# Kernel optimization log

Measured on AMD Instinct MI355X. Metric: run time of the kernel, lower is better.

## Reference

```python
import jax, jax.numpy as jnp
import numpy as np

B, C_LEN, Q_LEN, H = 32, 1024, 128, 512
NEG = -1e30  # effectively -inf for fp32 softmax


def setup_inputs() -> dict:
    key = jax.random.key(0)
    k1, k2, k3, k4, k5, k6 = jax.random.split(key, 6)
    C = jax.random.normal(k1, (B, C_LEN, H), dtype=jnp.float32)
    Q = jax.random.normal(k2, (B, Q_LEN, H), dtype=jnp.float32)
    C_mask = jax.random.randint(k3, (B, C_LEN), 0, 2, dtype=jnp.int32)
    Q_mask = jax.random.randint(k4, (B, Q_LEN), 0, 2, dtype=jnp.int32)
    # nn.Linear(3H, 1): weight [1, 3H], bias [1]; store as flat vector + scalar
    w = jax.random.normal(k5, (3 * H,), dtype=jnp.float32) * (1.0 / np.sqrt(3 * H))
    b = jax.random.normal(k6, (1,), dtype=jnp.float32) * 0.01
    return {"C": C, "Q": Q, "C_mask": C_mask, "Q_mask": Q_mask, "w": w, "b": b}


def reference(C, Q, C_mask, Q_mask, w, b):
    h = C.shape[-1]
    w1, w2, w3 = w[:h], w[h:2 * h], w[2 * h:]
    # Trilinear score decomposition (same math as Linear on cat(C, Q, C*Q)):
    # S[b,i,j] = C_i.w1 + Q_j.w2 + (C_i*w3).Q_j + bias
    S = (C @ w1)[:, :, None] + (Q @ w2)[:, None, :] \
        + jnp.einsum('bih,bjh->bij', C * w3, Q) + b[0]
    S_row = jax.nn.softmax(jnp.where(Q_mask[:, None, :] == 0, NEG, S), axis=2)
    S_col = jax.nn.softmax(jnp.where(C_mask[:, :, None] == 0, NEG, S), axis=1)
    A = jnp.einsum('bij,bjh->bih', S_row, Q)                     # [B, c_len, H]
    Bm = jnp.einsum('bij,bkj,bkh->bih', S_row, S_col, C)         # S_row @ S_col^T @ C
    return jnp.concatenate((C, A, C * A, C * Bm), axis=-1)       # [B, c_len, 4H]
```

## Files before the change

### kernel.cpp

```cpp
#include <hip/hip_runtime.h>
#include <hip/hip_bf16.h>
#include <math.h>

#define Bn 32
#define CL 1024
#define QL 128
#define Hh 512
#define NEGV (-1e30f)

typedef short bf16x8 __attribute__((ext_vector_type(8)));
typedef float f32x4 __attribute__((ext_vector_type(4)));

__device__ inline unsigned short f2bf(float x) {
  union { float f; unsigned u; } v; v.f = x;
  unsigned r = v.u + 0x7fff + ((v.u >> 16) & 1);
  return (unsigned short)(r >> 16);
}
__device__ inline unsigned packbf(float x, float y) {
  return (unsigned)f2bf(x) | ((unsigned)f2bf(y) << 16);
}

__global__ __launch_bounds__(256) void rowdot_kernel(
    const float* __restrict__ X, const float* __restrict__ w,
    const float* __restrict__ bias, float* __restrict__ out, int nrows) {
  int row = blockIdx.x * 4 + (threadIdx.x >> 6);
  int lane = threadIdx.x & 63;
  if (row >= nrows) return;
  const float* x = X + (size_t)row * Hh;
  float s = 0.f;
  for (int h = lane; h < Hh; h += 64) s += x[h] * w[h];
  for (int off = 32; off > 0; off >>= 1) s += __shfl_down(s, off, 64);
  if (lane == 0) out[row] = s + (bias ? bias[0] : 0.f);
}

__global__ __launch_bounds__(256) void prep_q_kernel(
    const float* __restrict__ Q, unsigned short* __restrict__ QT) {
  __shared__ float tile[QL * 65];
  int b = blockIdx.y, h0 = blockIdx.x * 64, t = threadIdx.x;
  const float* Qb = Q + (size_t)b * QL * Hh;
  unsigned* QTu = (unsigned*)QT + ((size_t)b * Hh + h0) * (QL / 2);
  for (int l = 0; l < 16; ++l) {
    int idx = t + l * 256; int c = idx & 31, j = idx >> 5;
    float2 v = *(const float2*)(Qb + (size_t)j * Hh + h0 + 2 * c);
    tile[j * 65 + 2 * c] = v.x;
    tile[j * 65 + 2 * c + 1] = v.y;
  }
  __syncthreads();
  for (int l = 0; l < 16; ++l) {
    int idx = t + l * 256; int jc = idx & 63, h = idx >> 6;
    QTu[(size_t)h * (QL / 2) + jc] =
        packbf(tile[(2 * jc) * 65 + h], tile[(2 * jc + 1) * 65 + h]);
  }
}

__global__ __launch_bounds__(256) void s_mfma_kernel(
    const float* __restrict__ C, const float* __restrict__ Q,
    const float* __restrict__ w3, const int* __restrict__ Qmask,
    const float* __restrict__ rc, const float* __restrict__ cq,
    float* __restrict__ S, unsigned short* __restrict__ Prow) {
  __shared__ unsigned sA[64 * 16];
  __shared__ unsigned sB[128 * 16];
  __shared__ float sW[Hh];
  __shared__ int qm[QL];
  int b = blockIdx.y, i0 = blockIdx.x * 64, t = threadIdx.x;
  if (t < QL) qm[t] = Qmask[b * QL + t];
  for (int l = t; l < Hh; l += 256) sW[l] = w3[l];
  __syncthreads();
  int lane = t & 63, w = t >> 6;
  int lanen = lane & 15, quad = lane >> 4;
  f32x4 acc[8];
  for (int nt = 0; nt < 8; ++nt) acc[nt] = (f32x4){0.f, 0.f, 0.f, 0.f};
  const float* Cb = C + ((size_t)b * CL + i0) * Hh;
  const float* Qb = Q + (size_t)b * QL * Hh;
  for (int k0 = 0; k0 < Hh; k0 += 32) {
    for (int l = 0; l < 4; ++l) {
      int idx = t + l * 256; int c = idx & 15, rr = idx >> 4;
      float2 v = *(const float2*)(Cb + (size_t)rr * Hh + k0 + c * 2);
      sA[rr * 16 + c] = packbf(v.x * sW[k0 + c * 2], v.y * sW[k0 + c * 2 + 1]);
    }
    for (int l = 0; l < 8; ++l) {
      int idx = t + l * 256; int c = idx & 15, j = idx >> 4;
      float2 v = *(const float2*)(Qb + (size_t)j * Hh + k0 + c * 2);
      sB[j * 16 + c] = packbf(v.x, v.y);
    }
    __syncthreads();
    bf16x8 a = *(const bf16x8*)(sA + (w * 16 + lanen) * 16 + quad * 4);
    for (int nt = 0; nt < 8; ++nt) {
      bf16x8 bb = *(const bf16x8*)(sB + (nt * 16 + lanen) * 16 + quad * 4);
      acc[nt] = __builtin_amdgcn_mfma_f32_16x16x32_bf16(a, bb, acc[nt], 0, 0, 0);
    }
    __syncthreads();
  }
  float cqv[8]; int qmv[8];
  for (int nt = 0; nt < 8; ++nt) {
    int j = nt * 16 + lanen;
    cqv[nt] = cq[b * QL + j]; qmv[nt] = qm[j];
  }
  int rowbase = i0 + w * 16 + quad * 4;
  for (int r = 0; r < 4; ++r) {
    int row = rowbase + r;
    float rcv = rc[b * CL + row];
    float vals[8], mv = -INFINITY;
    for (int nt = 0; nt < 8; ++nt) {
      float val = acc[nt][r] + rcv + cqv[nt];
      vals[nt] = val;
      mv = fmaxf(mv, qmv[nt] ? val : NEGV);
    }
    for (int off = 1; off < 16; off <<= 1) mv = fmaxf(mv, __shfl_xor(mv, off, 64));
    float ls = 0.f;
    for (int nt = 0; nt < 8; ++nt) ls += __expf((qmv[nt] ? vals[nt] : NEGV) - mv);
    for (int off = 1; off < 16; off <<= 1) ls += __shfl_xor(ls, off, 64);
    float linv = 1.f / ls;
    size_t base = ((size_t)b * CL + row) * QL;
    for (int nt = 0; nt < 8; ++nt) {
      int j = nt * 16 + lanen;
      S[base + j] = vals[nt];
      Prow[base + j] = f2bf(__expf((qmv[nt] ? vals[nt] : NEGV) - mv) * linv);
    }
  }
}

__global__ __launch_bounds__(256) void colstat1_kernel(
    const float* __restrict__ S, const int* __restrict__ Cmask,
    float* __restrict__ partm, float* __restrict__ partl) {
  __shared__ int cm[64];
  __shared__ float sm[QL], sl[QL];
  int b = blockIdx.y, chunk = blockIdx.x, t = threadIdx.x;
  int i0 = chunk * 64;
  if (t < 64) cm[t] = Cmask[b * CL + i0 + t];
  __syncthreads();
  int j = t & 127, ir = t >> 7;
  float m = -INFINITY, l = 0.f;
  const float* Sb = S + ((size_t)b * CL + i0) * QL;
  for (int i = ir; i < 64; i += 2) {
    float v = cm[i] ? Sb[(size_t)i * QL + j] : NEGV;
    float nm = fmaxf(m, v);
    l = l * __expf(m - nm) + __expf(v - nm);
    m = nm;
  }
  if (ir == 1) { sm[j] = m; sl[j] = l; }
  __syncthreads();
  if (ir == 0) {
    float m2 = sm[j], l2 = sl[j];
    float nm = fmaxf(m, m2);
    float L = l * __expf(m - nm) + l2 * __expf(m2 - nm);
    partm[(b * 16 + chunk) * QL + j] = nm;
    partl[(b * 16 + chunk) * QL + j] = L;
  }
}

__global__ __launch_bounds__(128) void colstat2_kernel(
    const float* __restrict__ partm, const float* __restrict__ partl,
    float* __restrict__ colm, float* __restrict__ colinv) {
  int b = blockIdx.x, j = threadIdx.x;
  float m = -INFINITY, L = 0.f;
  for (int c = 0; c < 16; ++c) {
    float m2 = partm[(b * 16 + c) * QL + j], l2 = partl[(b * 16 + c) * QL + j];
    float nm = fmaxf(m, m2);
    L = L * __expf(m - nm) + l2 * __expf(m2 - nm);
    m = nm;
  }
  colm[b * QL + j] = m;
  colinv[b * QL + j] = 1.f / L;
}

__global__ __launch_bounds__(256) void pcol_kernel(
    const float* __restrict__ S, const int* __restrict__ Cmask,
    const float* __restrict__ colm, const float* __restrict__ colinv,
    unsigned short* __restrict__ PT) {
  __shared__ float tile[64 * 129];
  __shared__ int cm[64];
  __shared__ float cmj[QL], civ[QL];
  int b = blockIdx.y, i0 = blockIdx.x * 64, t = threadIdx.x;
  if (t < 64) cm[t] = Cmask[b * CL + i0 + t];
  if (t >= 128) { int j = t - 128; cmj[j] = colm[b * QL + j]; civ[j] = colinv[b * QL + j]; }
  __syncthreads();
  const float* Sb = S + ((size_t)b * CL + i0) * QL;
  for (int l = 0; l < 32; ++l) {
    int idx = t + l * 256; int j = idx & 127, il = idx >> 7;
    float v = cm[il] ? Sb[(size_t)il * QL + j] : NEGV;
    tile[il * 129 + j] = __expf(v - cmj[j]) * civ[j];
  }
  __syncthreads();
  unsigned* PTu = (unsigned*)PT;
  for (int l = 0; l < 16; ++l) {
    int idx = t + l * 256; int c = idx & 31, j = idx >> 5;
    PTu[(((size_t)b * QL + j) * CL + i0) / 2 + c] =
        packbf(tile[(2 * c) * 129 + j], tile[(2 * c + 1) * 129 + j]);
  }
}

__global__ __launch_bounds__(256) void t_mfma_kernel(
    const float* __restrict__ C, const unsigned short* __restrict__ PT,
    unsigned short* __restrict__ TT) {
  __shared__ float ftile[32 * 33];
  __shared__ unsigned sA[32 * 16];
  __shared__ unsigned sB[128 * 16];
  int b = blockIdx.y, h0 = blockIdx.x * 32, t = threadIdx.x;
  int lane = t & 63, w = t >> 6;
  int lanen = lane & 15, quad = lane >> 4;
  int mw = w >> 1, nw = w & 1;
  f32x4 acc[4];
  for (int nt = 0; nt < 4; ++nt) acc[nt] = (f32x4){0.f, 0.f, 0.f, 0.f};
  const float* Cb = C + (size_t)b * CL * Hh;
  const unsigned* PTu = (const unsigned*)PT + ((size_t)b * QL * CL) / 2;
  for (int i0 = 0; i0 < CL; i0 += 32) {
    for (int l = 0; l < 4; ++l) {
      int idx = t + l * 256; int hh = idx & 31, ii = idx >> 5;
      ftile[ii * 33 + hh] = Cb[(size_t)(i0 + ii) * Hh + h0 + hh];
    }
    for (int l = 0; l < 8; ++l) {
      int idx = t + l * 256; int c = idx & 15, j = idx >> 4;
      sB[j * 16 + c] = PTu[(size_t)j * (CL / 2) + i0 / 2 + c];
    }
    __syncthreads();
    for (int l = 0; l < 2; ++l) {
      int idx = t + l * 256; int c = idx & 15, hh = idx >> 4;
      sA[hh * 16 + c] = packbf(ftile[(2 * c) * 33 + hh], ftile[(2 * c + 1) * 33 + hh]);
    }
    __syncthreads();
    bf16x8 a = *(const bf16x8*)(sA + (mw * 16 + lanen) * 16 + quad * 4);
    for (int nt = 0; nt < 4; ++nt) {
      bf16x8 bb = *(const bf16x8*)(sB + (nw * 64 + nt * 16 + lanen) * 16 + quad * 4);
      acc[nt] = __builtin_amdgcn_mfma_f32_16x16x32_bf16(a, bb, acc[nt], 0, 0, 0);
    }
    __syncthreads();
  }
  for (int nt = 0; nt < 4; ++nt)
    for (int r = 0; r < 4; ++r) {
      int h = h0 + mw * 16 + quad * 4 + r;
      int j = nw * 64 + nt * 16 + lanen;
      TT[((size_t)b * Hh + h) * QL + j] = f2bf(acc[nt][r]);
    }
}

__global__ __launch_bounds__(256) void out_mfma_kernel(
    const unsigned short* __restrict__ Prow, const unsigned short* __restrict__ TT,
    const unsigned short* __restrict__ QT, const float* __restrict__ C,
    float* __restrict__ out) {
  __shared__ unsigned smem[3 * 64 * 64];
  unsigned* sP = smem;
  unsigned* sQ = smem + 64 * 64;
  unsigned* sT = smem + 2 * 64 * 64;
  int b = blockIdx.z, i0 = blockIdx.y * 64, h0 = blockIdx.x * 64, t = threadIdx.x;
  int lane = t & 63, w = t >> 6;
  int lanen = lane & 15, quad = lane >> 4;
  const unsigned* Pu = (const unsigned*)Prow + ((size_t)b * CL + i0) * (QL / 2);
  const unsigned* Tu = (const unsigned*)TT + ((size_t)b * Hh + h0) * (QL / 2);
  const unsigned* Qu = (const unsigned*)QT + ((size_t)b * Hh + h0) * (QL / 2);
  for (int l = 0; l < 16; ++l) {
    int idx = t + l * 256; int c = idx & 63, rr = idx >> 6;
    int cs = c ^ ((rr & 7) << 2);
    sP[rr * 64 + cs] = Pu[(size_t)rr * 64 + c];
    sQ[rr * 64 + cs] = Qu[(size_t)rr * 64 + c];
    sT[rr * 64 + cs] = Tu[(size_t)rr * 64 + c];
  }
  __syncthreads();
  f32x4 accA[4], accB[4];
  for (int nt = 0; nt < 4; ++nt) {
    accA[nt] = (f32x4){0.f, 0.f, 0.f, 0.f};
    accB[nt] = (f32x4){0.f, 0.f, 0.f, 0.f};
  }
  for (int kk = 0; kk < 4; ++kk) {
    int arow = w * 16 + lanen;
    bf16x8 a = *(const bf16x8*)(sP + arow * 64 + ((kk * 16 + quad * 4) ^ ((arow & 7) << 2)));
    for (int nt = 0; nt < 4; ++nt) {
      int brow = nt * 16 + lanen;
      int boff = brow * 64 + ((kk * 16 + quad * 4) ^ ((brow & 7) << 2));
      bf16x8 bq = *(const bf16x8*)(sQ + boff);
      bf16x8 bt = *(const bf16x8*)(sT + boff);
      accA[nt] = __builtin_amdgcn_mfma_f32_16x16x32_bf16(a, bq, accA[nt], 0, 0, 0);
      accB[nt] = __builtin_amdgcn_mfma_f32_16x16x32_bf16(a, bt, accB[nt], 0, 0, 0);
    }
  }
  __syncthreads();
  float* fA = (float*)smem;
  float* fB = (float*)smem + 64 * 65;
  for (int nt = 0; nt < 4; ++nt)
    for (int r = 0; r < 4; ++r) {
      int iL = w * 16 + quad * 4 + r;
      int hL = nt * 16 + lanen;
      fA[iL * 65 + hL] = accA[nt][r];
      fB[iL * 65 + hL] = accB[nt][r];
    }
  __syncthreads();
  for (int rr = 0; rr < 16; ++rr) {
    int iL = w * 16 + rr;
    int i = i0 + iL;
    const float* Crow = C + ((size_t)b * CL + i) * Hh + h0;
    float* orow = out + ((size_t)b * CL + i) * (size_t)(4 * Hh) + h0;
    float cv = Crow[lane];
    float av = fA[iL * 65 + lane];
    float bv = fB[iL * 65 + lane];
    orow[lane] = cv;
    orow[Hh + lane] = av;
    orow[2 * Hh + lane] = cv * av;
    orow[3 * Hh + lane] = cv * bv;
  }
}

extern "C" void kernel_launch(void* const* d_in, const int* in_sizes, int n_in,
                              void* d_out, int out_size, void* d_ws, size_t ws_size,
                              hipStream_t stream) {
  const float* C = (const float*)d_in[0];
  const float* Q = (const float*)d_in[1];
  const int* Cmask = (const int*)d_in[2];
  const int* Qmask = (const int*)d_in[3];
  const float* w = (const float*)d_in[4];
  const float* bptr = (const float*)d_in[5];
  float* out = (float*)d_out;
  float* f = (float*)d_ws;

  float* rc     = f;
  float* cq     = f + 32768;
  float* colm   = f + 36864;
  float* colinv = f + 40960;
  float* partm  = f + 45056;
  float* partl  = f + 110592;
  float* S      = f + 176128;
  unsigned short* Prow = (unsigned short*)(f + 4370432);
  unsigned short* PT   = Prow + 4194304;
  unsigned short* TT   = PT + 4194304;
  unsigned short* QT   = TT + 2097152;

  rowdot_kernel<<<dim3((Bn * CL) / 4), 256, 0, stream>>>(C, w, nullptr, rc, Bn * CL);
  rowdot_kernel<<<dim3((Bn * QL) / 4), 256, 0, stream>>>(Q, w + Hh, bptr, cq, Bn * QL);
  prep_q_kernel<<<dim3(Hh / 64, Bn), 256, 0, stream>>>(Q, QT);
  s_mfma_kernel<<<dim3(CL / 64, Bn), 256, 0, stream>>>(C, Q, w + 2 * Hh, Qmask, rc, cq, S, Prow);
  colstat1_kernel<<<dim3(16, Bn), 256, 0, stream>>>(S, Cmask, partm, partl);
  colstat2_kernel<<<dim3(Bn), 128, 0, stream>>>(partm, partl, colm, colinv);
  pcol_kernel<<<dim3(CL / 64, Bn), 256, 0, stream>>>(S, Cmask, colm, colinv, PT);
  t_mfma_kernel<<<dim3(Hh / 32, Bn), 256, 0, stream>>>(C, PT, TT);
  out_mfma_kernel<<<dim3(Hh / 64, CL / 64, Bn), 256, 0, stream>>>(Prow, TT, QT, C, out);
}
```

Before: 481.1 us.

## Pre-transpose C to bf16 and widen t_mfma K-tile with swizzled LDS

```diff
diff --git a/kernel.cpp b/kernel.cpp
--- a/kernel.cpp
+++ b/kernel.cpp
@@ -50,6 +50,28 @@
     int idx = t + l * 256; int jc = idx & 63, h = idx >> 6;
     QTu[(size_t)h * (QL / 2) + jc] =
         packbf(tile[(2 * jc) * 65 + h], tile[(2 * jc + 1) * 65 + h]);
+  }
+}
+
+__global__ __launch_bounds__(256) void prep_ct_kernel(
+    const float* __restrict__ C, unsigned short* __restrict__ CT16) {
+  __shared__ float tile[64 * 65];
+  int b = blockIdx.y, t = threadIdx.x;
+  int i0 = (blockIdx.x & 15) * 64;
+  int h0 = (blockIdx.x >> 4) * 64;
+  const float* Cb = C + ((size_t)b * CL + i0) * Hh;
+  for (int l = 0; l < 8; ++l) {
+    int idx = t + l * 256; int c = idx & 31, i = idx >> 5;
+    float2 v = *(const float2*)(Cb + (size_t)i * Hh + h0 + 2 * c);
+    tile[i * 65 + 2 * c] = v.x;
+    tile[i * 65 + 2 * c + 1] = v.y;
+  }
+  __syncthreads();
+  unsigned* CTu = (unsigned*)CT16 + ((size_t)b * Hh + h0) * (CL / 2) + i0 / 2;
+  for (int l = 0; l < 8; ++l) {
+    int idx = t + l * 256; int ip = idx & 31, h = idx >> 5;
+    CTu[(size_t)h * (CL / 2) + ip] =
+        packbf(tile[(2 * ip) * 65 + h], tile[(2 * ip + 1) * 65 + h]);
   }
 }
 
@@ -191,38 +213,36 @@
 }
 
 __global__ __launch_bounds__(256) void t_mfma_kernel(
-    const float* __restrict__ C, const unsigned short* __restrict__ PT,
+    const unsigned short* __restrict__ CT16, const unsigned short* __restrict__ PT,
     unsigned short* __restrict__ TT) {
-  __shared__ float ftile[32 * 33];
-  __shared__ unsigned sA[32 * 16];
-  __shared__ unsigned sB[128 * 16];
+  __shared__ unsigned sA[32 * 32];
+  __shared__ unsigned sB[128 * 32];
   int b = blockIdx.y, h0 = blockIdx.x * 32, t = threadIdx.x;
   int lane = t & 63, w = t >> 6;
   int lanen = lane & 15, quad = lane >> 4;
   int mw = w >> 1, nw = w & 1;
   f32x4 acc[4];
   for (int nt = 0; nt < 4; ++nt) acc[nt] = (f32x4){0.f, 0.f, 0.f, 0.f};
-  const float* Cb = C + (size_t)b * CL * Hh;
-  const unsigned* PTu = (const unsigned*)PT + ((size_t)b * QL * CL) / 2;
-  for (int i0 = 0; i0 < CL; i0 += 32) {
+  const unsigned* CTu = (const unsigned*)CT16 + ((size_t)b * Hh + h0) * (CL / 2);
+  const unsigned* PTu = (const unsigned*)PT + (size_t)b * QL * (CL / 2);
+  for (int i0 = 0; i0 < CL; i0 += 64) {
     for (int l = 0; l < 4; ++l) {
-      int idx = t + l * 256; int hh = idx & 31, ii = idx >> 5;
-      ftile[ii * 33 + hh] = Cb[(size_t)(i0 + ii) * Hh + h0 + hh];
-    }
-    for (int l = 0; l < 8; ++l) {
-      int idx = t + l * 256; int c = idx & 15, j = idx >> 4;
-      sB[j * 16 + c] = PTu[(size_t)j * (CL / 2) + i0 / 2 + c];
+      int idx = t + l * 256; int c = idx & 31, hh = idx >> 5;
+      sA[hh * 32 + (c ^ ((hh & 7) << 2))] = CTu[(size_t)hh * (CL / 2) + i0 / 2 + c];
+    }
+    for (int l = 0; l < 16; ++l) {
+      int idx = t + l * 256; int c = idx & 31, j = idx >> 5;
+      sB[j * 32 + (c ^ ((j & 7) << 2))] = PTu[(size_t)j * (CL / 2) + i0 / 2 + c];
     }
     __syncthreads();
-    for (int l = 0; l < 2; ++l) {
-      int idx = t + l * 256; int c = idx & 15, hh = idx >> 4;
-      sA[hh * 16 + c] = packbf(ftile[(2 * c) * 33 + hh], ftile[(2 * c + 1) * 33 + hh]);
-    }
-    __syncthreads();
-    bf16x8 a = *(const bf16x8*)(sA + (mw * 16 + lanen) * 16 + quad * 4);
-    for (int nt = 0; nt < 4; ++nt) {
-      bf16x8 bb = *(const bf16x8*)(sB + (nw * 64 + nt * 16 + lanen) * 16 + quad * 4);
-      acc[nt] = __builtin_amdgcn_mfma_f32_16x16x32_bf16(a, bb, acc[nt], 0, 0, 0);
+    for (int kk = 0; kk < 2; ++kk) {
+      int arow = mw * 16 + lanen;
+      bf16x8 a = *(const bf16x8*)(sA + arow * 32 + ((kk * 16 + quad * 4) ^ ((arow & 7) << 2)));
+      for (int nt = 0; nt < 4; ++nt) {
+        int brow = nw * 64 + nt * 16 + lanen;
+        bf16x8 bb = *(const bf16x8*)(sB + brow * 32 + ((kk * 16 + quad * 4) ^ ((brow & 7) << 2)));
+        acc[nt] = __builtin_amdgcn_mfma_f32_16x16x32_bf16(a, bb, acc[nt], 0, 0, 0);
+      }
     }
     __syncthreads();
   }
@@ -322,14 +342,16 @@
   unsigned short* PT   = Prow + 4194304;
   unsigned short* TT   = PT + 4194304;
   unsigned short* QT   = TT + 2097152;
+  unsigned short* CT16 = QT + 2097152;
 
   rowdot_kernel<<<dim3((Bn * CL) / 4), 256, 0, stream>>>(C, w, nullptr, rc, Bn * CL);
   rowdot_kernel<<<dim3((Bn * QL) / 4), 256, 0, stream>>>(Q, w + Hh, bptr, cq, Bn * QL);
   prep_q_kernel<<<dim3(Hh / 64, Bn), 256, 0, stream>>>(Q, QT);
+  prep_ct_kernel<<<dim3(16 * (Hh / 64), Bn), 256, 0, stream>>>(C, CT16);
   s_mfma_kernel<<<dim3(CL / 64, Bn), 256, 0, stream>>>(C, Q, w + 2 * Hh, Qmask, rc, cq, S, Prow);
   colstat1_kernel<<<dim3(16, Bn), 256, 0, stream>>>(S, Cmask, partm, partl);
   colstat2_kernel<<<dim3(Bn), 128, 0, stream>>>(partm, partl, colm, colinv);
   pcol_kernel<<<dim3(CL / 64, Bn), 256, 0, stream>>>(S, Cmask, colm, colinv, PT);
-  t_mfma_kernel<<<dim3(Hh / 32, Bn), 256, 0, stream>>>(C, PT, TT);
+  t_mfma_kernel<<<dim3(Hh / 32, Bn), 256, 0, stream>>>(CT16, PT, TT);
   out_mfma_kernel<<<dim3(Hh / 64, CL / 64, Bn), 256, 0, stream>>>(Prow, TT, QT, C, out);
 }
```

Result: slower. 569.1 us (+18.3%).
